# Kernel optimization log

Measured on AMD Instinct MI355X. Metric: run time of the kernel, lower is better.

The kernel has to match this reference:

```python
import jax, jax.numpy as jnp
import numpy as np

B, T, D, H, L, F = 32, 512, 1024, 1024, 2, 256  # batch, time, input dim, units, layers, feature_size


def setup_inputs() -> dict:
    key = jax.random.key(0)
    ks = jax.random.split(key, 9)
    s_in = 1.0 / np.sqrt(D)
    s_h = 1.0 / np.sqrt(H)
    x = jax.random.normal(ks[0], (B, T, D), dtype=jnp.float32)
    # Stacked LSTM params: gate order [i, f, g, o] concatenated along last axis.
    Wx = jax.random.normal(ks[1], (L, D, 4 * H), dtype=jnp.float32) * s_in
    Wh = jax.random.normal(ks[2], (L, H, 4 * H), dtype=jnp.float32) * s_h
    b = jnp.zeros((L, 4 * H), dtype=jnp.float32)
    # Output heads.
    Wmu = jax.random.normal(ks[3], (H, F), dtype=jnp.float32) * s_h
    bmu = jnp.zeros((F,), dtype=jnp.float32)
    Wls = jax.random.normal(ks[4], (H, F), dtype=jnp.float32) * s_h
    bls = jnp.zeros((F,), dtype=jnp.float32)
    y_min = jnp.zeros((F,), dtype=jnp.float32)  # y_min init arg (0.0 broadcast)
    return {"x": x, "Wx": Wx, "Wh": Wh, "b": b, "Wmu": Wmu, "bmu": bmu,
            "Wls": Wls, "bls": bls, "y_min": y_min}


def _lstm_layer(x, Wx, Wh, b):
    # x: [B, T, Din]; Wx: [Din, 4H]; Wh: [H, 4H]; b: [4H]
    Bn = x.shape[0]
    Hn = Wh.shape[0]
    # Precompute input projections for all timesteps (one big GEMM).
    x_proj = jnp.einsum('btd,dg->btg', x, Wx) + b  # [B, T, 4H]

    def step(carry, xp):
        h, c = carry
        g = xp + h @ Wh  # [B, 4H]
        i, f, gg, o = jnp.split(g, 4, axis=-1)
        c = jax.nn.sigmoid(f) * c + jax.nn.sigmoid(i) * jnp.tanh(gg)
        h = jax.nn.sigmoid(o) * jnp.tanh(c)
        return (h, c), h

    h0 = jnp.zeros((Bn, Hn), dtype=x.dtype)
    c0 = jnp.zeros((Bn, Hn), dtype=x.dtype)
    _, hs = jax.lax.scan(step, (h0, c0), jnp.swapaxes(x_proj, 0, 1))  # hs: [T, B, H]
    return jnp.swapaxes(hs, 0, 1)  # [B, T, H]


def reference(x, Wx, Wh, b, Wmu, bmu, Wls, bls, y_min):
    for l in range(Wx.shape[0]):  # small fixed n_layers loop
        x = _lstm_layer(x, Wx[l], Wh[l], b[l])
    mu = jax.nn.softplus(x @ Wmu + bmu) + y_min  # [B, T, F]
    log_sigma = x @ Wls + bls                    # [B, T, F]
    return (mu, log_sigma)
```

## Files before the change

kernel.cpp:

```cpp
#include <hip/hip_runtime.h>

typedef unsigned short u16;
typedef unsigned int   u32;
typedef unsigned long long u64;
typedef short s16x4 __attribute__((ext_vector_type(4)));
typedef short s16x8 __attribute__((ext_vector_type(8)));
typedef float f32x4 __attribute__((ext_vector_type(4)));
typedef u32   u32x4 __attribute__((ext_vector_type(4)));

#define GK 1024

__device__ inline u16 f2bf(float f) {
    u32 u = __builtin_bit_cast(u32, f);
    u += 0x7FFFu + ((u >> 16) & 1u);
    return (u16)(u >> 16);
}
__device__ inline u16 f2h(float f) {
    _Float16 h = (_Float16)f;
    return __builtin_bit_cast(u16, h);
}
__device__ inline float h2f(u16 u) {
    return (float)__builtin_bit_cast(_Float16, u);
}
__device__ inline float fast_sigmoid(float x) {
    return __builtin_amdgcn_rcpf(1.f + __expf(-x));
}
__device__ inline float fast_tanh(float x) {
    return 1.f - 2.f * __builtin_amdgcn_rcpf(1.f + __expf(2.f * x));
}
__device__ inline f32x4 mfma16(s16x8 a, s16x8 b, f32x4 c) {
    return __builtin_amdgcn_mfma_f32_16x16x32_bf16(a, b, c, 0, 0, 0);
}
__device__ inline s16x8 mk8(s16x4 lo, s16x4 hi) {
    return __builtin_shufflevector(lo, hi, 0, 1, 2, 3, 4, 5, 6, 7);
}

__global__ void k_f2bf(const float* __restrict__ in, u16* __restrict__ out, int n) {
    int i = (blockIdx.x * 256 + threadIdx.x) * 4;
    if (i < n) {
        float4 v = *(const float4*)(in + i);
        ushort4 o;
        o.x = f2bf(v.x); o.y = f2bf(v.y); o.z = f2bf(v.z); o.w = f2bf(v.w);
        *(ushort4*)(out + i) = o;
    }
}

__global__ void k_transpose_bf(const float* __restrict__ in, u16* __restrict__ out,
                               int R, int C) {
    __shared__ float tile[32][33];
    int tid = threadIdx.x;
    int xs = (tid & 7) * 4;
    int y  = tid >> 3;
    int r0 = blockIdx.y * 32, c0 = blockIdx.x * 32;
    float4 v = *(const float4*)(in + (size_t)(r0 + y) * C + c0 + xs);
    tile[y][xs + 0] = v.x; tile[y][xs + 1] = v.y;
    tile[y][xs + 2] = v.z; tile[y][xs + 3] = v.w;
    __syncthreads();
    ushort4 o;
    o.x = f2bf(tile[xs + 0][y]); o.y = f2bf(tile[xs + 1][y]);
    o.z = f2bf(tile[xs + 2][y]); o.w = f2bf(tile[xs + 3][y]);
    *(ushort4*)(out + (size_t)(c0 + y) * R + r0 + xs) = o;
}

__global__ void k_wpackip(u16* __restrict__ wm) {
    int idx = blockIdx.x * 256 + threadIdx.x;
    u64* p = (u64*)(wm + (size_t)idx * 32);
    u64 w0 = p[0], w1 = p[1], w2 = p[2], w3 = p[3];
    u64 w4 = p[4], w5 = p[5], w6 = p[6], w7 = p[7];
    p[0] = w0; p[1] = w4; p[2] = w1; p[3] = w5;
    p[4] = w2; p[5] = w6; p[6] = w3; p[7] = w7;
}

__global__ void k_unpack(const u16* __restrict__ in, u16* __restrict__ out) {
    int idx = blockIdx.x * 256 + threadIdx.x;
    int slot = idx >> 12;
    int c = idx & 4095;
    int q = c >> 7, b = (c >> 2) & 31, ri = c & 3;
    const u16* p = in + (size_t)(slot + 1) * 32768 + q * 1024 + b * 32 + ri * 8;
    u64 lo = *(const u64*)p;
    u64 hi = *(const u64*)(p + 4);
    u16* o = out + (size_t)(slot * 32 + b) * 1024 + q * 32 + ri * 4;
    *(u64*)o = lo;
    *(u64*)(o + 16) = hi;
}

template<int MODE>
__launch_bounds__(256, 2)
__global__ void k_gemm(const u16* __restrict__ A, const u16* __restrict__ BT,
                       const float* __restrict__ bias,
                       u16* __restrict__ Cb, float* __restrict__ Cf,
                       const float* __restrict__ b2, const float* __restrict__ ymin,
                       int gridN) {
    int bid = blockIdx.x;
    int m0 = (bid / gridN) * 128, n0 = (bid % gridN) * 128;
    __shared__ u16 As[128 * 40];
    __shared__ u16 Bs[128 * 40];
    int tid = threadIdx.x;
    int lane = tid & 63, w = tid >> 6;
    int wr = w >> 1, wc = w & 1;
    int rr = lane & 15, r16 = lane >> 4;
    f32x4 acc[4][4] = {};
    for (int kt = 0; kt < GK / 32; ++kt) {
        int k0 = kt * 32;
#pragma unroll
        for (int it = 0; it < 2; ++it) {
            int idx = it * 256 + tid;
            int row = idx >> 2, ch = idx & 3;
            *(u32x4*)(&As[row * 40 + ch * 8]) =
                *(const u32x4*)(A + (size_t)(m0 + row) * GK + k0 + ch * 8);
            *(u32x4*)(&Bs[row * 40 + ch * 8]) =
                *(const u32x4*)(BT + (size_t)(n0 + row) * GK + k0 + ch * 8);
        }
        __syncthreads();
        s16x8 af[4], bfr[4];
#pragma unroll
        for (int i = 0; i < 4; ++i) {
            int abase = (wr * 64 + i * 16 + rr) * 40 + r16 * 4;
            af[i] = mk8(*(const s16x4*)(&As[abase]), *(const s16x4*)(&As[abase + 16]));
            int bbase = (wc * 64 + i * 16 + rr) * 40 + r16 * 4;
            bfr[i] = mk8(*(const s16x4*)(&Bs[bbase]), *(const s16x4*)(&Bs[bbase + 16]));
        }
#pragma unroll
        for (int i = 0; i < 4; ++i)
#pragma unroll
            for (int j = 0; j < 4; ++j)
                acc[i][j] = mfma16(af[i], bfr[j], acc[i][j]);
        __syncthreads();
    }
#pragma unroll
    for (int i = 0; i < 4; ++i) {
#pragma unroll
        for (int j = 0; j < 4; ++j) {
#pragma unroll
            for (int r = 0; r < 4; ++r) {
                int m = m0 + wr * 64 + i * 16 + r16 * 4 + r;
                int n = n0 + wc * 64 + j * 16 + rr;
                float v = acc[i][j][r];
                if (MODE == 0) {
                    v += bias[n];
                    int orow = (m & 511) * 32 + (m >> 9);
                    int colx = ((n & 1023) << 2) | (n >> 10);
                    Cb[(size_t)orow * 4096 + colx] = f2h(v);
                } else {
                    int orow = (m & 31) * 512 + (m >> 5);
                    if (n < 256) {
                        v += bias[n];
                        float sp = fmaxf(v, 0.f) + log1pf(expf(-fabsf(v)));
                        Cf[(size_t)orow * 256 + n] = sp + ymin[n];
                    } else {
                        v += b2[n - 256];
                        Cf[4194304 + (size_t)orow * 256 + (n - 256)] = v;
                    }
                }
            }
        }
    }
}

__device__ inline float lstm_core(f32x4 acc, float ai, float af, float ag, float ao,
                                  float& c, int lane) {
    float r0 = acc[0], r1 = acc[1], r2 = acc[2], r3 = acc[3];
    float x0 = __shfl_xor(r0, 1), x1 = __shfl_xor(r1, 1);
    float x2 = __shfl_xor(r2, 1), x3 = __shfl_xor(r3, 1);
    bool o1 = lane & 1;
    float s0 = o1 ? x1 : r0, s1 = o1 ? r1 : x0;
    float s2 = o1 ? x3 : r2, s3 = o1 ? r3 : x2;
    float y0 = __shfl_xor(s0, 2), y1 = __shfl_xor(s1, 2);
    float y2 = __shfl_xor(s2, 2), y3 = __shfl_xor(s3, 2);
    bool o2 = lane & 2;
    float gi = (o2 ? y2 : s0) + ai;
    float gf = (o2 ? y3 : s1) + af;
    float gg = (o2 ? s2 : y0) + ag;
    float go = (o2 ? s3 : y1) + ao;
    float I  = fast_sigmoid(gi);
    float Fg = fast_sigmoid(gf);
    float G  = fast_tanh(gg);
    float O  = fast_sigmoid(go);
    c = Fg * c + I * G;
    return O * fast_tanh(c);
}
__device__ inline void pack_plain(float h, int lane, u16* dst) {
    u32 hq = (u32)f2bf(h);
    u32 o4 = (u32)__shfl_xor((int)hq, 4);
    u32 m32 = (lane & 4) ? ((o4 & 0xffffu) | (hq << 16))
                         : ((hq & 0xffffu) | (o4 << 16));
    u32 o8 = (u32)__shfl_xor((int)m32, 8);
    u64 m64 = (lane & 8) ? (((u64)o8) | ((u64)m32 << 32))
                         : (((u64)m32) | ((u64)o8 << 32));
    if ((lane & 12) == 0) *(u64*)dst = m64;
}
__device__ inline int e0_of(int base) {
    return ((base & 15) >> 2) * 8 + ((base >> 4) & 1) * 4;
}

__launch_bounds__(256, 1)
__global__ void k_step(int t,
                       const u16* __restrict__ Wp0, const u16* __restrict__ Wpx,
                       const u16* __restrict__ Wp1, const u16* __restrict__ xproj,
                       const float* __restrict__ b1,
                       u16* __restrict__ hbuf0, u16* __restrict__ hseq1,
                       float* __restrict__ c0buf, float* __restrict__ c1buf) {
    __shared__ f32x4 part[2][2][2][64];
    int tid = threadIdx.x, bid = blockIdx.x;
    int lane = tid & 63, w = tid >> 6;
    int mt = w & 1, qh = w >> 1;
    int rr = lane & 15, r16 = lane >> 4;
    int b_ = mt * 16 + ((lane >> 4) << 2) + (lane & 3);
    int uu = (lane >> 2) & 3;
    const int cb = mt * 512 + rr * 32 + r16 * 8;

    if (bid < 128) {
        if (t >= 512) return;
        int blk = bid;
        size_t cg0 = (size_t)((rr & 3) * 1024 + blk * 8 + (rr >> 2));
        const u16* w0 = Wp0 + cg0 * GK + qh * 512 + r16 * 8;
        const u16* w1 = Wp0 + (cg0 + 4) * GK + qh * 512 + r16 * 8;
        const u16* hp = hbuf0 + (size_t)(t & 1) * 32768 + qh * 16384 + cb;
        u32x4 hf[16];
#pragma unroll
        for (int j = 0; j < 16; ++j) hf[j] = *(const u32x4*)(hp + j * 1024);
        f32x4 a0 = {}, a1 = {};
#pragma unroll
        for (int j = 0; j < 16; ++j) {
            s16x8 a = __builtin_bit_cast(s16x8, hf[j]);
            a0 = mfma16(a, *(const s16x8*)(w0 + j * 32), a0);
            a1 = mfma16(a, *(const s16x8*)(w1 + j * 32), a1);
        }
        part[mt][1 - qh][0][lane] = qh ? a0 : a1;
        __syncthreads();
        f32x4 acc = (qh ? a1 : a0) + part[mt][qh][0][lane];
        int unit = blk * 8 + qh * 4 + uu;
        u64 xv = *(const u64*)(xproj + (size_t)(t * 32 + b_) * 4096 + unit * 4);
        float c = c0buf[b_ * 1024 + unit];
        float h = lstm_core(acc, h2f((u16)xv), h2f((u16)(xv >> 16)),
                            h2f((u16)(xv >> 32)), h2f((u16)(xv >> 48)), c, lane);
        c0buf[b_ * 1024 + unit] = c;
        int E0 = e0_of((blk & 3) * 8 + qh * 4);
        u16* dst = hbuf0 + (size_t)((t + 1) & 1) * 32768 + (blk >> 2) * 1024
                 + b_ * 32 + E0;
        pack_plain(h, lane, dst);
    } else {
        if (t < 1) return;
        int blk = bid - 128;
        size_t cg0 = (size_t)((rr & 3) * 1024 + blk * 8 + (rr >> 2));
        size_t woff = qh * 512 + r16 * 8;
        const u16* wh0 = Wp1 + cg0 * GK + woff;
        const u16* wh1 = Wp1 + (cg0 + 4) * GK + woff;
        const u16* wx0 = Wpx + cg0 * GK + woff;
        const u16* wx1 = Wpx + (cg0 + 4) * GK + woff;
        const u16* hp1 = hseq1 + (size_t)(t - 1) * 32768 + qh * 16384 + cb;
        const u16* hp0 = hbuf0 + (size_t)(t & 1) * 32768 + qh * 16384 + cb;
        u32x4 hf[16], gfr[16];
#pragma unroll
        for (int j = 0; j < 16; ++j) hf[j] = *(const u32x4*)(hp1 + j * 1024);
#pragma unroll
        for (int j = 0; j < 16; ++j) gfr[j] = *(const u32x4*)(hp0 + j * 1024);
        f32x4 aH0 = {}, aH1 = {}, aX0 = {}, aX1 = {};
#pragma unroll
        for (int j = 0; j < 16; ++j) {
            s16x8 a = __builtin_bit_cast(s16x8, hf[j]);
            aH0 = mfma16(a, *(const s16x8*)(wh0 + j * 32), aH0);
            aH1 = mfma16(a, *(const s16x8*)(wh1 + j * 32), aH1);
            s16x8 g = __builtin_bit_cast(s16x8, gfr[j]);
            aX0 = mfma16(g, *(const s16x8*)(wx0 + j * 32), aX0);
            aX1 = mfma16(g, *(const s16x8*)(wx1 + j * 32), aX1);
        }
        part[mt][1 - qh][0][lane] = qh ? aH0 : aH1;
        part[mt][1 - qh][1][lane] = qh ? aX0 : aX1;
        __syncthreads();
        f32x4 acc = (qh ? aH1 : aH0) + (qh ? aX1 : aX0)
                  + part[mt][qh][0][lane] + part[mt][qh][1][lane];
        int unit = blk * 8 + qh * 4 + uu;
        float c = c1buf[b_ * 1024 + unit];
        float h = lstm_core(acc, b1[unit], b1[1024 + unit], b1[2048 + unit],
                            b1[3072 + unit], c, lane);
        c1buf[b_ * 1024 + unit] = c;
        int E0 = e0_of((blk & 3) * 8 + qh * 4);
        u16* dst = hseq1 + (size_t)t * 32768 + (blk >> 2) * 1024 + b_ * 32 + E0;
        pack_plain(h, lane, dst);
    }
}

extern "C" void kernel_launch(void* const* d_in, const int* in_sizes, int n_in,
                              void* d_out, int out_size, void* d_ws, size_t ws_size,
                              hipStream_t stream) {
    const float* x   = (const float*)d_in[0];
    const float* Wx  = (const float*)d_in[1];
    const float* Wh  = (const float*)d_in[2];
    const float* b   = (const float*)d_in[3];
    const float* Wmu = (const float*)d_in[4];
    const float* bmu = (const float*)d_in[5];
    const float* Wls = (const float*)d_in[6];
    const float* bls = (const float*)d_in[7];
    const float* ym  = (const float*)d_in[8];
    float* out = (float*)d_out;

    char* ws = (char*)d_ws;
    u16*   xbf   = (u16*)(ws);
    u16*   hbuf0 = (u16*)(ws);
    float* c0buf = (float*)(ws + 131072);
    float* c1buf = (float*)(ws + 262144);
    u16*   wxT   = (u16*)(ws + 33554432);
    u16*   whT   = (u16*)(ws + 50331648);
    u16*   whdT  = (u16*)(ws + 67108864);
    u16*   xproj = (u16*)(ws + 68157440);
    u16*   h1lin = xproj;
    u16*   hseq1 = (u16*)(ws + 202375168);

    k_f2bf<<<16384, 256, 0, stream>>>(x, xbf, 16777216);
    dim3 tg(128, 32);
    k_transpose_bf<<<tg, 256, 0, stream>>>(Wx,           wxT,           1024, 4096);
    k_transpose_bf<<<tg, 256, 0, stream>>>(Wx + 4194304, wxT + 4194304, 1024, 4096);
    k_transpose_bf<<<tg, 256, 0, stream>>>(Wh,           whT,           1024, 4096);
    k_transpose_bf<<<tg, 256, 0, stream>>>(Wh + 4194304, whT + 4194304, 1024, 4096);
    dim3 hg(8, 32);
    k_transpose_bf<<<hg, 256, 0, stream>>>(Wmu, whdT,          1024, 256);
    k_transpose_bf<<<hg, 256, 0, stream>>>(Wls, whdT + 262144, 1024, 256);

    k_gemm<0><<<4096, 256, 0, stream>>>(xbf, wxT, b, xproj, nullptr, nullptr, nullptr, 32);

    k_wpackip<<<1024, 256, 0, stream>>>(whT);
    k_wpackip<<<512, 256, 0, stream>>>(wxT + 4194304);

    hipMemsetAsync(hbuf0, 0, 65536, stream);
    hipMemsetAsync(c0buf, 0, 262144, stream);
    hipMemsetAsync(hseq1, 0, 65536, stream);

    for (int t = 0; t <= 512; ++t)
        k_step<<<256, 256, 0, stream>>>(t, whT, wxT + 4194304, whT + 4194304, xproj,
                                        b + 4096, hbuf0, hseq1, c0buf, c1buf);

    k_unpack<<<8192, 256, 0, stream>>>(hseq1, h1lin);
    k_gemm<1><<<512, 256, 0, stream>>>(h1lin, whdT, bmu, nullptr, out, bls, ym, 4);
}
```

Before: 6.673 ms.

## Fuse input bf16 conversion into GEMM and merge layer step blocks

Drops the standalone fp32-to-bf16 pass over x and converts x to bf16 inside the xproj GEMM's shared-memory tile load, saving one full write and read of the 32MB bf16 copy. The per-timestep kernel changes from 256 blocks of 256 threads to 128 blocks of 512 threads, with layer-0 and layer-1 work for the same unit slice sharing one block and one barrier. This halves the block count per launch across 513 sequential launches. The trade-offs are scalar 2-byte shared stores in the GEMM loader and larger blocks, where the layer-0 half may idle while waiting for the layer-1 half.

```diff
diff --git a/kernel.cpp b/kernel.cpp
--- a/kernel.cpp
+++ b/kernel.cpp
@@ -33,16 +33,6 @@
 }
 __device__ inline s16x8 mk8(s16x4 lo, s16x4 hi) {
     return __builtin_shufflevector(lo, hi, 0, 1, 2, 3, 4, 5, 6, 7);
-}
-
-__global__ void k_f2bf(const float* __restrict__ in, u16* __restrict__ out, int n) {
-    int i = (blockIdx.x * 256 + threadIdx.x) * 4;
-    if (i < n) {
-        float4 v = *(const float4*)(in + i);
-        ushort4 o;
-        o.x = f2bf(v.x); o.y = f2bf(v.y); o.z = f2bf(v.z); o.w = f2bf(v.w);
-        *(ushort4*)(out + i) = o;
-    }
 }
 
 __global__ void k_transpose_bf(const float* __restrict__ in, u16* __restrict__ out,
@@ -86,7 +76,8 @@
 
 template<int MODE>
 __launch_bounds__(256, 2)
-__global__ void k_gemm(const u16* __restrict__ A, const u16* __restrict__ BT,
+__global__ void k_gemm(const u16* __restrict__ A, const float* __restrict__ Af,
+                       const u16* __restrict__ BT,
                        const float* __restrict__ bias,
                        u16* __restrict__ Cb, float* __restrict__ Cf,
                        const float* __restrict__ b2, const float* __restrict__ ymin,
@@ -106,8 +97,19 @@
         for (int it = 0; it < 2; ++it) {
             int idx = it * 256 + tid;
             int row = idx >> 2, ch = idx & 3;
-            *(u32x4*)(&As[row * 40 + ch * 8]) =
-                *(const u32x4*)(A + (size_t)(m0 + row) * GK + k0 + ch * 8);
+            if (MODE == 0) {
+                const float* ap = Af + (size_t)(m0 + row) * GK + k0 + ch * 8;
+                float4 vlo = *(const float4*)ap;
+                float4 vhi = *(const float4*)(ap + 4);
+                u16* d = &As[row * 40 + ch * 8];
+                d[0] = f2bf(vlo.x); d[1] = f2bf(vlo.y);
+                d[2] = f2bf(vlo.z); d[3] = f2bf(vlo.w);
+                d[4] = f2bf(vhi.x); d[5] = f2bf(vhi.y);
+                d[6] = f2bf(vhi.z); d[7] = f2bf(vhi.w);
+            } else {
+                *(u32x4*)(&As[row * 40 + ch * 8]) =
+                    *(const u32x4*)(A + (size_t)(m0 + row) * GK + k0 + ch * 8);
+            }
             *(u32x4*)(&Bs[row * 40 + ch * 8]) =
                 *(const u32x4*)(BT + (size_t)(n0 + row) * GK + k0 + ch * 8);
         }
@@ -193,91 +195,98 @@
     return ((base & 15) >> 2) * 8 + ((base >> 4) & 1) * 4;
 }
 
-__launch_bounds__(256, 1)
+__launch_bounds__(512, 2)
 __global__ void k_step(int t,
                        const u16* __restrict__ Wp0, const u16* __restrict__ Wpx,
                        const u16* __restrict__ Wp1, const u16* __restrict__ xproj,
                        const float* __restrict__ b1,
                        u16* __restrict__ hbuf0, u16* __restrict__ hseq1,
                        float* __restrict__ c0buf, float* __restrict__ c1buf) {
-    __shared__ f32x4 part[2][2][2][64];
-    int tid = threadIdx.x, bid = blockIdx.x;
+    __shared__ f32x4 part0[2][2][64];
+    __shared__ f32x4 part1[2][2][2][64];
+    int tid = threadIdx.x, blk = blockIdx.x;
     int lane = tid & 63, w = tid >> 6;
-    int mt = w & 1, qh = w >> 1;
+    int isL1 = w >> 2, wl = w & 3;
+    int mt = wl & 1, qh = wl >> 1;
     int rr = lane & 15, r16 = lane >> 4;
     int b_ = mt * 16 + ((lane >> 4) << 2) + (lane & 3);
     int uu = (lane >> 2) & 3;
     const int cb = mt * 512 + rr * 32 + r16 * 8;
-
-    if (bid < 128) {
-        if (t >= 512) return;
-        int blk = bid;
-        size_t cg0 = (size_t)((rr & 3) * 1024 + blk * 8 + (rr >> 2));
-        const u16* w0 = Wp0 + cg0 * GK + qh * 512 + r16 * 8;
-        const u16* w1 = Wp0 + (cg0 + 4) * GK + qh * 512 + r16 * 8;
-        const u16* hp = hbuf0 + (size_t)(t & 1) * 32768 + qh * 16384 + cb;
-        u32x4 hf[16];
-#pragma unroll
-        for (int j = 0; j < 16; ++j) hf[j] = *(const u32x4*)(hp + j * 1024);
-        f32x4 a0 = {}, a1 = {};
-#pragma unroll
-        for (int j = 0; j < 16; ++j) {
-            s16x8 a = __builtin_bit_cast(s16x8, hf[j]);
-            a0 = mfma16(a, *(const s16x8*)(w0 + j * 32), a0);
-            a1 = mfma16(a, *(const s16x8*)(w1 + j * 32), a1);
-        }
-        part[mt][1 - qh][0][lane] = qh ? a0 : a1;
-        __syncthreads();
-        f32x4 acc = (qh ? a1 : a0) + part[mt][qh][0][lane];
-        int unit = blk * 8 + qh * 4 + uu;
-        u64 xv = *(const u64*)(xproj + (size_t)(t * 32 + b_) * 4096 + unit * 4);
-        float c = c0buf[b_ * 1024 + unit];
-        float h = lstm_core(acc, h2f((u16)xv), h2f((u16)(xv >> 16)),
-                            h2f((u16)(xv >> 32)), h2f((u16)(xv >> 48)), c, lane);
-        c0buf[b_ * 1024 + unit] = c;
-        int E0 = e0_of((blk & 3) * 8 + qh * 4);
-        u16* dst = hbuf0 + (size_t)((t + 1) & 1) * 32768 + (blk >> 2) * 1024
-                 + b_ * 32 + E0;
-        pack_plain(h, lane, dst);
+    size_t cg0 = (size_t)((rr & 3) * 1024 + blk * 8 + (rr >> 2));
+    size_t woff = qh * 512 + r16 * 8;
+
+    f32x4 v0 = {}, v1 = {}, v2 = {}, v3 = {};
+    if (!isL1) {
+        if (t < 512) {
+            const u16* w0 = Wp0 + cg0 * GK + woff;
+            const u16* w1 = Wp0 + (cg0 + 4) * GK + woff;
+            const u16* hp = hbuf0 + (size_t)(t & 1) * 32768 + qh * 16384 + cb;
+            u32x4 hf[16];
+#pragma unroll
+            for (int j = 0; j < 16; ++j) hf[j] = *(const u32x4*)(hp + j * 1024);
+#pragma unroll
+            for (int j = 0; j < 16; ++j) {
+                s16x8 a = __builtin_bit_cast(s16x8, hf[j]);
+                v0 = mfma16(a, *(const s16x8*)(w0 + j * 32), v0);
+                v1 = mfma16(a, *(const s16x8*)(w1 + j * 32), v1);
+            }
+            part0[mt][1 - qh][lane] = qh ? v0 : v1;
+        }
     } else {
-        if (t < 1) return;
-        int blk = bid - 128;
-        size_t cg0 = (size_t)((rr & 3) * 1024 + blk * 8 + (rr >> 2));
-        size_t woff = qh * 512 + r16 * 8;
-        const u16* wh0 = Wp1 + cg0 * GK + woff;
-        const u16* wh1 = Wp1 + (cg0 + 4) * GK + woff;
-        const u16* wx0 = Wpx + cg0 * GK + woff;
-        const u16* wx1 = Wpx + (cg0 + 4) * GK + woff;
-        const u16* hp1 = hseq1 + (size_t)(t - 1) * 32768 + qh * 16384 + cb;
-        const u16* hp0 = hbuf0 + (size_t)(t & 1) * 32768 + qh * 16384 + cb;
-        u32x4 hf[16], gfr[16];
-#pragma unroll
-        for (int j = 0; j < 16; ++j) hf[j] = *(const u32x4*)(hp1 + j * 1024);
-#pragma unroll
-        for (int j = 0; j < 16; ++j) gfr[j] = *(const u32x4*)(hp0 + j * 1024);
-        f32x4 aH0 = {}, aH1 = {}, aX0 = {}, aX1 = {};
-#pragma unroll
-        for (int j = 0; j < 16; ++j) {
-            s16x8 a = __builtin_bit_cast(s16x8, hf[j]);
-            aH0 = mfma16(a, *(const s16x8*)(wh0 + j * 32), aH0);
-            aH1 = mfma16(a, *(const s16x8*)(wh1 + j * 32), aH1);
-            s16x8 g = __builtin_bit_cast(s16x8, gfr[j]);
-            aX0 = mfma16(g, *(const s16x8*)(wx0 + j * 32), aX0);
-            aX1 = mfma16(g, *(const s16x8*)(wx1 + j * 32), aX1);
-        }
-        part[mt][1 - qh][0][lane] = qh ? aH0 : aH1;
-        part[mt][1 - qh][1][lane] = qh ? aX0 : aX1;
-        __syncthreads();
-        f32x4 acc = (qh ? aH1 : aH0) + (qh ? aX1 : aX0)
-                  + part[mt][qh][0][lane] + part[mt][qh][1][lane];
-        int unit = blk * 8 + qh * 4 + uu;
-        float c = c1buf[b_ * 1024 + unit];
-        float h = lstm_core(acc, b1[unit], b1[1024 + unit], b1[2048 + unit],
-                            b1[3072 + unit], c, lane);
-        c1buf[b_ * 1024 + unit] = c;
-        int E0 = e0_of((blk & 3) * 8 + qh * 4);
-        u16* dst = hseq1 + (size_t)t * 32768 + (blk >> 2) * 1024 + b_ * 32 + E0;
-        pack_plain(h, lane, dst);
+        if (t >= 1) {
+            const u16* wh0 = Wp1 + cg0 * GK + woff;
+            const u16* wh1 = Wp1 + (cg0 + 4) * GK + woff;
+            const u16* wx0 = Wpx + cg0 * GK + woff;
+            const u16* wx1 = Wpx + (cg0 + 4) * GK + woff;
+            const u16* hp1 = hseq1 + (size_t)(t - 1) * 32768 + qh * 16384 + cb;
+            const u16* hp0 = hbuf0 + (size_t)(t & 1) * 32768 + qh * 16384 + cb;
+            u32x4 hf[16], gfr[16];
+#pragma unroll
+            for (int j = 0; j < 16; ++j) hf[j] = *(const u32x4*)(hp1 + j * 1024);
+#pragma unroll
+            for (int j = 0; j < 16; ++j) gfr[j] = *(const u32x4*)(hp0 + j * 1024);
+#pragma unroll
+            for (int j = 0; j < 16; ++j) {
+                s16x8 a = __builtin_bit_cast(s16x8, hf[j]);
+                v0 = mfma16(a, *(const s16x8*)(wh0 + j * 32), v0);
+                v1 = mfma16(a, *(const s16x8*)(wh1 + j * 32), v1);
+                s16x8 g = __builtin_bit_cast(s16x8, gfr[j]);
+                v2 = mfma16(g, *(const s16x8*)(wx0 + j * 32), v2);
+                v3 = mfma16(g, *(const s16x8*)(wx1 + j * 32), v3);
+            }
+            part1[mt][1 - qh][0][lane] = qh ? v0 : v1;
+            part1[mt][1 - qh][1][lane] = qh ? v2 : v3;
+        }
+    }
+    __syncthreads();
+
+    if (!isL1) {
+        if (t < 512) {
+            f32x4 acc = (qh ? v1 : v0) + part0[mt][qh][lane];
+            int unit = blk * 8 + qh * 4 + uu;
+            u64 xv = *(const u64*)(xproj + (size_t)(t * 32 + b_) * 4096 + unit * 4);
+            float c = c0buf[b_ * 1024 + unit];
+            float h = lstm_core(acc, h2f((u16)xv), h2f((u16)(xv >> 16)),
+                                h2f((u16)(xv >> 32)), h2f((u16)(xv >> 48)), c, lane);
+            c0buf[b_ * 1024 + unit] = c;
+            int E0 = e0_of((blk & 3) * 8 + qh * 4);
+            u16* dst = hbuf0 + (size_t)((t + 1) & 1) * 32768 + (blk >> 2) * 1024
+                     + b_ * 32 + E0;
+            pack_plain(h, lane, dst);
+        }
+    } else {
+        if (t >= 1) {
+            f32x4 acc = (qh ? v1 : v0) + (qh ? v3 : v2)
+                      + part1[mt][qh][0][lane] + part1[mt][qh][1][lane];
+            int unit = blk * 8 + qh * 4 + uu;
+            float c = c1buf[b_ * 1024 + unit];
+            float h = lstm_core(acc, b1[unit], b1[1024 + unit], b1[2048 + unit],
+                                b1[3072 + unit], c, lane);
+            c1buf[b_ * 1024 + unit] = c;
+            int E0 = e0_of((blk & 3) * 8 + qh * 4);
+            u16* dst = hseq1 + (size_t)t * 32768 + (blk >> 2) * 1024 + b_ * 32 + E0;
+            pack_plain(h, lane, dst);
+        }
     }
 }
 
@@ -296,7 +305,6 @@
     float* out = (float*)d_out;
 
     char* ws = (char*)d_ws;
-    u16*   xbf   = (u16*)(ws);
     u16*   hbuf0 = (u16*)(ws);
     float* c0buf = (float*)(ws + 131072);
     float* c1buf = (float*)(ws + 262144);
@@ -307,7 +315,6 @@
     u16*   h1lin = xproj;
     u16*   hseq1 = (u16*)(ws + 202375168);
 
-    k_f2bf<<<16384, 256, 0, stream>>>(x, xbf, 16777216);
     dim3 tg(128, 32);
     k_transpose_bf<<<tg, 256, 0, stream>>>(Wx,           wxT,           1024, 4096);
     k_transpose_bf<<<tg, 256, 0, stream>>>(Wx + 4194304, wxT + 4194304, 1024, 4096);
@@ -317,7 +324,8 @@
     k_transpose_bf<<<hg, 256, 0, stream>>>(Wmu, whdT,          1024, 256);
     k_transpose_bf<<<hg, 256, 0, stream>>>(Wls, whdT + 262144, 1024, 256);
 
-    k_gemm<0><<<4096, 256, 0, stream>>>(xbf, wxT, b, xproj, nullptr, nullptr, nullptr, 32);
+    k_gemm<0><<<4096, 256, 0, stream>>>(nullptr, x, wxT, b, xproj,
+                                        nullptr, nullptr, nullptr, 32);
 
     k_wpackip<<<1024, 256, 0, stream>>>(whT);
     k_wpackip<<<512, 256, 0, stream>>>(wxT + 4194304);
@@ -327,9 +335,10 @@
     hipMemsetAsync(hseq1, 0, 65536, stream);
 
     for (int t = 0; t <= 512; ++t)
-        k_step<<<256, 256, 0, stream>>>(t, whT, wxT + 4194304, whT + 4194304, xproj,
+        k_step<<<128, 512, 0, stream>>>(t, whT, wxT + 4194304, whT + 4194304, xproj,
                                         b + 4096, hbuf0, hseq1, c0buf, c1buf);
 
     k_unpack<<<8192, 256, 0, stream>>>(hseq1, h1lin);
-    k_gemm<1><<<512, 256, 0, stream>>>(h1lin, whdT, bmu, nullptr, out, bls, ym, 4);
-}
+    k_gemm<1><<<512, 256, 0, stream>>>(h1lin, nullptr, whdT, bmu, nullptr, out,
+                                       bls, ym, 4);
+}
```

Measured after the change: 8.939 ms. 34.0% more time.
